# Performance work log

Measured on AMD Instinct MI355X. Metric: run time of the kernel, lower is better.

## Reference

```python
import jax, jax.numpy as jnp
import numpy as np
import math

NUM_BUCKETS = 32
MAX_DISTANCE = 128
NUM_HEADS = 16
D_MODEL = 1024
HEAD_DIM = D_MODEL // NUM_HEADS


def _relative_position_bucket(relative_position, num_buckets=NUM_BUCKETS, max_distance=MAX_DISTANCE):
    # bidirectional=False path of the original
    rp = -jnp.minimum(relative_position, 0)  # non-negative distances
    max_exact = num_buckets // 2
    is_small = rp < max_exact
    rp_safe = jnp.maximum(rp, 1).astype(jnp.float32)
    rp_if_large = max_exact + (
        jnp.log(rp_safe / max_exact) / math.log(max_distance / max_exact) * (num_buckets - max_exact)
    ).astype(jnp.int32)
    rp_if_large = jnp.minimum(rp_if_large, num_buckets - 1)
    return jnp.where(is_small, rp, rp_if_large)


def relative_bias(rab_weight, q_len, k_len):
    ctx = jnp.arange(q_len)[:, None]
    mem = jnp.arange(k_len)[None, :]
    buckets = _relative_position_bucket(mem - ctx)  # [Q, K]
    vals = rab_weight[buckets]                       # [Q, K, H]
    return jnp.transpose(vals, (2, 0, 1))[None]      # [1, H, Q, K]


def setup_inputs() -> dict:
    key = jax.random.key(0)
    k1, k2, k3, k4 = jax.random.split(key, 4)
    B, S = 4, 2048
    return {
        "v": jax.random.normal(k1, (B, S, D_MODEL), dtype=jnp.float32),
        "k": jax.random.normal(k2, (B, S, D_MODEL), dtype=jnp.float32),
        "q": jax.random.normal(k3, (B, S, D_MODEL), dtype=jnp.float32),
        "rab_weight": jax.random.normal(k4, (NUM_BUCKETS, NUM_HEADS), dtype=jnp.float32),
    }


def reference(v, k, q, rab_weight):
    B, S, _ = q.shape
    def split(x):
        return jnp.transpose(x.reshape(B, S, NUM_HEADS, HEAD_DIM), (0, 2, 1, 3))  # [B,H,S,D]
    qh, kh, vh = split(q), split(k), split(v)
    scores = jnp.einsum("bhqd,bhkd->bhqk", qh, kh)          # [B,H,S,S]
    scores = scores + relative_bias(rab_weight, S, S)        # add relative bias
    av = jnp.einsum("bhqk,bhkd->bhqd", jax.nn.silu(scores), vh)
    return jnp.transpose(av, (0, 2, 1, 3)).reshape(B, S, D_MODEL)
```

## Files before the change

### kernel.cpp

```cpp
#include <hip/hip_runtime.h>

#define SEQ 2048
#define NH 16
#define HD 64
#define DMODEL 1024

typedef short bf16x8 __attribute__((ext_vector_type(8)));
typedef float f32x16 __attribute__((ext_vector_type(16)));

union FragU {
    bf16x8 v;
    uint2 u2[2];
    unsigned int w[4];
    unsigned short s[8];
};

#if __has_builtin(__builtin_amdgcn_cvt_pk_bf16_f32)
typedef __bf16 v2bf_t __attribute__((ext_vector_type(2)));
__device__ __forceinline__ unsigned int pack_bf16(float lo, float hi) {
    union { v2bf_t h; unsigned int u; } cv;
    cv.h = __builtin_amdgcn_cvt_pk_bf16_f32(lo, hi);
    return cv.u;
}
#else
__device__ __forceinline__ unsigned int pack_bf16(float lo, float hi) {
    unsigned int a = __float_as_uint(lo) + 0x8000u;
    unsigned int b = __float_as_uint(hi) + 0x8000u;
    return __builtin_amdgcn_perm(b, a, 0x07060302);
}
#endif

#define EXP_SCALE 1.44269504f
#define LN2       0.69314718f

__global__ __launch_bounds__(512, 4)
void paa_kernel(const float* __restrict__ Vg, const float* __restrict__ Kg,
                const float* __restrict__ Qg, const float* __restrict__ RW,
                float* __restrict__ Og)
{
    __shared__ __align__(16) unsigned short KsLds[2][64 * 68];
    __shared__ __align__(16) unsigned short VtLds[2][64 * 68];
    __shared__ float btab[128];

    const int tid  = threadIdx.x;
    const int lane = tid & 63;
    const int wave = tid >> 6;
    const int half = lane >> 5;
    const int l31  = lane & 31;

    const int bid  = blockIdx.x;
    const int bh   = bid & 63;
    const int qt   = bid >> 6;
    const int b    = bh >> 4;
    const int head = bh & 15;

    const int q0w = qt * 256 + wave * 32;

    if (tid < 128) {
        int rp = tid;
        int bucket;
        if (rp < 16) bucket = rp;
        else {
            int big = 16 + (int)(logf((float)rp * 0.0625f) * 7.6943736f);
            bucket = big < 31 ? big : 31;
        }
        btab[tid] = RW[bucket * NH + head] * EXP_SCALE;
    }

    FragU qf[4];
    {
        const float* qrow = Qg + (size_t)(b * SEQ + q0w + l31) * DMODEL + head * HD;
        #pragma unroll
        for (int kf = 0; kf < 4; ++kf) {
            int dd = kf * 16 + half * 8;
            float4 x0 = *(const float4*)(qrow + dd);
            float4 x1 = *(const float4*)(qrow + dd + 4);
            FragU f;
            f.w[0] = pack_bf16(x0.x * EXP_SCALE, x0.y * EXP_SCALE);
            f.w[1] = pack_bf16(x0.z * EXP_SCALE, x0.w * EXP_SCALE);
            f.w[2] = pack_bf16(x1.x * EXP_SCALE, x1.y * EXP_SCALE);
            f.w[3] = pack_bf16(x1.z * EXP_SCALE, x1.w * EXP_SCALE);
            qf[kf] = f;
        }
    }

    f32x16 oacc[2];
    #pragma unroll
    for (int n = 0; n < 2; ++n)
        #pragma unroll
        for (int r = 0; r < 16; ++r) oacc[n][r] = 0.0f;

    const int krow = tid >> 4;
    const int c4   = tid & 15;
    const int kc2  = tid >> 4;
    const int d4   = tid & 15;

    const float* kp = Kg + (size_t)(b * SEQ + krow) * DMODEL + head * HD + c4 * 4;
    const float* vp = Vg + (size_t)(b * SEQ + kc2 * 2) * DMODEL + head * HD + d4 * 4;

    {
        float4 k0 = *(const float4*)(kp);
        float4 k1 = *(const float4*)(kp + (size_t)32 * DMODEL);
        float4 v0 = *(const float4*)(vp);
        float4 v1 = *(const float4*)(vp + DMODEL);
        kp += (size_t)64 * DMODEL;
        vp += (size_t)64 * DMODEL;
        uint2 w;
        w.x = pack_bf16(k0.x, k0.y); w.y = pack_bf16(k0.z, k0.w);
        *(uint2*)&KsLds[0][krow * 68 + c4 * 4] = w;
        w.x = pack_bf16(k1.x, k1.y); w.y = pack_bf16(k1.z, k1.w);
        *(uint2*)&KsLds[0][(krow + 32) * 68 + c4 * 4] = w;
        *(unsigned int*)&VtLds[0][(d4 * 4 + 0) * 68 + kc2 * 2] = pack_bf16(v0.x, v1.x);
        *(unsigned int*)&VtLds[0][(d4 * 4 + 1) * 68 + kc2 * 2] = pack_bf16(v0.y, v1.y);
        *(unsigned int*)&VtLds[0][(d4 * 4 + 2) * 68 + kc2 * 2] = pack_bf16(v0.z, v1.z);
        *(unsigned int*)&VtLds[0][(d4 * 4 + 3) * 68 + kc2 * 2] = pack_bf16(v0.w, v1.w);
    }
    __syncthreads();

    const float bias_d0  = btab[0];
    const float bias_far = btab[127];

    #pragma unroll 2
    for (int it = 0; it < 32; ++it) {
        const int cur = it & 1;
        const int kcb = it * 64;
        const unsigned short* Ks = KsLds[cur];
        const unsigned short* Vt = VtLds[cur];
        const bool pre = (it < 31);

        float4 k0, k1, v0, v1;
        if (pre) {
            k0 = *(const float4*)(kp);
            k1 = *(const float4*)(kp + (size_t)32 * DMODEL);
            v0 = *(const float4*)(vp);
            v1 = *(const float4*)(vp + DMODEL);
            kp += (size_t)64 * DMODEL;
            vp += (size_t)64 * DMODEL;
        }

        f32x16 st[2];
        #pragma unroll
        for (int t = 0; t < 2; ++t) {
            const int kcmin = kcb + t * 32;
            if (q0w + 31 - kcmin <= 0) {
                #pragma unroll
                for (int r = 0; r < 16; ++r) st[t][r] = bias_d0;
            } else if (q0w - (kcmin + 31) >= 113) {
                #pragma unroll
                for (int r = 0; r < 16; ++r) st[t][r] = bias_far;
            } else {
                const int dql = q0w + l31 - kcmin - 4 * half;
                #pragma unroll
                for (int r = 0; r < 16; ++r) {
                    int dv = dql - ((r & 3) + 8 * (r >> 2));
                    dv = dv < 0 ? 0 : (dv > 127 ? 127 : dv);
                    st[t][r] = btab[dv];
                }
            }
        }

        __builtin_amdgcn_s_setprio(1);
        #pragma unroll
        for (int kf = 0; kf < 4; ++kf) {
            FragU ka0, ka1;
            {
                int off = l31 * 68 + kf * 16 + half * 8;
                ka0.u2[0] = *(const uint2*)&Ks[off];
                ka0.u2[1] = *(const uint2*)&Ks[off + 4];
                off += 32 * 68;
                ka1.u2[0] = *(const uint2*)&Ks[off];
                ka1.u2[1] = *(const uint2*)&Ks[off + 4];
            }
            st[0] = __builtin_amdgcn_mfma_f32_32x32x16_bf16(ka0.v, qf[kf].v, st[0], 0, 0, 0);
            st[1] = __builtin_amdgcn_mfma_f32_32x32x16_bf16(ka1.v, qf[kf].v, st[1], 0, 0, 0);
        }
        __builtin_amdgcn_s_setprio(0);

        FragU pf0, pf1, pf2, pf3;
        {
            float vals[16];
            #pragma unroll
            for (int r = 0; r < 16; ++r) {
                float x = st[0][r];
                float e = __builtin_amdgcn_exp2f(-x);
                vals[r] = x * __builtin_amdgcn_rcpf(1.0f + e);
            }
            #pragma unroll
            for (int j = 0; j < 4; ++j) pf0.w[j] = pack_bf16(vals[2 * j], vals[2 * j + 1]);
            #pragma unroll
            for (int j = 0; j < 4; ++j) pf1.w[j] = pack_bf16(vals[8 + 2 * j], vals[9 + 2 * j]);
        }
        #pragma unroll
        for (int n = 0; n < 2; ++n) {
            FragU vf;
            int off = (n * 32 + l31) * 68 + half * 4;
            vf.u2[0] = *(const uint2*)&Vt[off];
            vf.u2[1] = *(const uint2*)&Vt[off + 8];
            oacc[n] = __builtin_amdgcn_mfma_f32_32x32x16_bf16(pf0.v, vf.v, oacc[n], 0, 0, 0);
        }
        #pragma unroll
        for (int n = 0; n < 2; ++n) {
            FragU vf;
            int off = (n * 32 + l31) * 68 + 16 + half * 4;
            vf.u2[0] = *(const uint2*)&Vt[off];
            vf.u2[1] = *(const uint2*)&Vt[off + 8];
            oacc[n] = __builtin_amdgcn_mfma_f32_32x32x16_bf16(pf1.v, vf.v, oacc[n], 0, 0, 0);
        }

        if (pre) {
            const int nb = cur ^ 1;
            uint2 w;
            w.x = pack_bf16(k0.x, k0.y); w.y = pack_bf16(k0.z, k0.w);
            *(uint2*)&KsLds[nb][krow * 68 + c4 * 4] = w;
            w.x = pack_bf16(k1.x, k1.y); w.y = pack_bf16(k1.z, k1.w);
            *(uint2*)&KsLds[nb][(krow + 32) * 68 + c4 * 4] = w;
            *(unsigned int*)&VtLds[nb][(d4 * 4 + 0) * 68 + kc2 * 2] = pack_bf16(v0.x, v1.x);
            *(unsigned int*)&VtLds[nb][(d4 * 4 + 1) * 68 + kc2 * 2] = pack_bf16(v0.y, v1.y);
            *(unsigned int*)&VtLds[nb][(d4 * 4 + 2) * 68 + kc2 * 2] = pack_bf16(v0.z, v1.z);
            *(unsigned int*)&VtLds[nb][(d4 * 4 + 3) * 68 + kc2 * 2] = pack_bf16(v0.w, v1.w);
        }

        {
            float vals[16];
            #pragma unroll
            for (int r = 0; r < 16; ++r) {
                float x = st[1][r];
                float e = __builtin_amdgcn_exp2f(-x);
                vals[r] = x * __builtin_amdgcn_rcpf(1.0f + e);
            }
            #pragma unroll
            for (int j = 0; j < 4; ++j) pf2.w[j] = pack_bf16(vals[2 * j], vals[2 * j + 1]);
            #pragma unroll
            for (int j = 0; j < 4; ++j) pf3.w[j] = pack_bf16(vals[8 + 2 * j], vals[9 + 2 * j]);
        }
        #pragma unroll
        for (int n = 0; n < 2; ++n) {
            FragU vf;
            int off = (n * 32 + l31) * 68 + 32 + half * 4;
            vf.u2[0] = *(const uint2*)&Vt[off];
            vf.u2[1] = *(const uint2*)&Vt[off + 8];
            oacc[n] = __builtin_amdgcn_mfma_f32_32x32x16_bf16(pf2.v, vf.v, oacc[n], 0, 0, 0);
        }
        #pragma unroll
        for (int n = 0; n < 2; ++n) {
            FragU vf;
            int off = (n * 32 + l31) * 68 + 48 + half * 4;
            vf.u2[0] = *(const uint2*)&Vt[off];
            vf.u2[1] = *(const uint2*)&Vt[off + 8];
            oacc[n] = __builtin_amdgcn_mfma_f32_32x32x16_bf16(pf3.v, vf.v, oacc[n], 0, 0, 0);
        }

        if (pre) __syncthreads();
    }

    float* obase = Og + (size_t)(b * SEQ) * DMODEL + head * HD;
    #pragma unroll
    for (int r = 0; r < 16; ++r) {
        int q = q0w + (r & 3) + 8 * (r >> 2) + 4 * half;
        float* orow = obase + (size_t)q * DMODEL;
        #pragma unroll
        for (int n = 0; n < 2; ++n)
            orow[n * 32 + l31] = oacc[n][r] * LN2;
    }
}

extern "C" void kernel_launch(void* const* d_in, const int* in_sizes, int n_in,
                              void* d_out, int out_size, void* d_ws, size_t ws_size,
                              hipStream_t stream) {
    const float* v  = (const float*)d_in[0];
    const float* k  = (const float*)d_in[1];
    const float* q  = (const float*)d_in[2];
    const float* rw = (const float*)d_in[3];
    float* out = (float*)d_out;
    paa_kernel<<<dim3(512), dim3(512), 0, stream>>>(v, k, q, rw, out);
}
```

Baseline: 219.8 us.

## Software-pipeline second score half across iterations with triple-buffered V tiles

Defers the SiLU and PV MFMAs for the second 32-key half of each tile to the start of the next iteration. A third V LDS buffer keeps the previous tile's V alive for that deferred work, and the barrier moves earlier. The aim is to overlap the QK MFMAs with the elementwise SiLU work and cut the serial dependency within an iteration. In exchange it uses more LDS and carries an extra accumulator across iterations, which may raise register pressure at the 512x4 launch bounds.

```diff
diff --git a/kernel.cpp b/kernel.cpp
--- a/kernel.cpp
+++ b/kernel.cpp
@@ -39,7 +39,7 @@
                 float* __restrict__ Og)
 {
     __shared__ __align__(16) unsigned short KsLds[2][64 * 68];
-    __shared__ __align__(16) unsigned short VtLds[2][64 * 68];
+    __shared__ __align__(16) unsigned short VtLds[3][64 * 68];
     __shared__ float btab[128];
 
     const int tid  = threadIdx.x;
@@ -120,12 +120,17 @@
     const float bias_d0  = btab[0];
     const float bias_far = btab[127];
 
+    const unsigned short* Kc = KsLds[0];
+    unsigned short*       Kn = &KsLds[1][0];
+    const unsigned short* Vprev = VtLds[2];
+    const unsigned short* Vc = VtLds[0];
+    unsigned short*       Vn = &VtLds[1][0];
+
+    f32x16 s1c;
+
     #pragma unroll 2
     for (int it = 0; it < 32; ++it) {
-        const int cur = it & 1;
         const int kcb = it * 64;
-        const unsigned short* Ks = KsLds[cur];
-        const unsigned short* Vt = VtLds[cur];
         const bool pre = (it < 31);
 
         float4 k0, k1, v0, v1;
@@ -138,23 +143,55 @@
             vp += (size_t)64 * DMODEL;
         }
 
-        f32x16 st[2];
+        if (it > 0) {
+            float vals[16];
+            #pragma unroll
+            for (int r = 0; r < 16; ++r) {
+                float x = s1c[r];
+                float e = __builtin_amdgcn_exp2f(-x);
+                vals[r] = x * __builtin_amdgcn_rcpf(1.0f + e);
+            }
+            FragU pfA, pfB;
+            #pragma unroll
+            for (int j = 0; j < 4; ++j) pfA.w[j] = pack_bf16(vals[2 * j], vals[2 * j + 1]);
+            #pragma unroll
+            for (int j = 0; j < 4; ++j) pfB.w[j] = pack_bf16(vals[8 + 2 * j], vals[9 + 2 * j]);
+            #pragma unroll
+            for (int n = 0; n < 2; ++n) {
+                FragU vf;
+                int off = (n * 32 + l31) * 68 + 32 + half * 4;
+                vf.u2[0] = *(const uint2*)&Vprev[off];
+                vf.u2[1] = *(const uint2*)&Vprev[off + 8];
+                oacc[n] = __builtin_amdgcn_mfma_f32_32x32x16_bf16(pfA.v, vf.v, oacc[n], 0, 0, 0);
+            }
+            #pragma unroll
+            for (int n = 0; n < 2; ++n) {
+                FragU vf;
+                int off = (n * 32 + l31) * 68 + 48 + half * 4;
+                vf.u2[0] = *(const uint2*)&Vprev[off];
+                vf.u2[1] = *(const uint2*)&Vprev[off + 8];
+                oacc[n] = __builtin_amdgcn_mfma_f32_32x32x16_bf16(pfB.v, vf.v, oacc[n], 0, 0, 0);
+            }
+        }
+
+        f32x16 s0;
         #pragma unroll
         for (int t = 0; t < 2; ++t) {
+            f32x16& st = t ? s1c : s0;
             const int kcmin = kcb + t * 32;
             if (q0w + 31 - kcmin <= 0) {
                 #pragma unroll
-                for (int r = 0; r < 16; ++r) st[t][r] = bias_d0;
+                for (int r = 0; r < 16; ++r) st[r] = bias_d0;
             } else if (q0w - (kcmin + 31) >= 113) {
                 #pragma unroll
-                for (int r = 0; r < 16; ++r) st[t][r] = bias_far;
+                for (int r = 0; r < 16; ++r) st[r] = bias_far;
             } else {
                 const int dql = q0w + l31 - kcmin - 4 * half;
                 #pragma unroll
                 for (int r = 0; r < 16; ++r) {
                     int dv = dql - ((r & 3) + 8 * (r >> 2));
                     dv = dv < 0 ? 0 : (dv > 127 ? 127 : dv);
-                    st[t][r] = btab[dv];
+                    st[r] = btab[dv];
                 }
             }
         }
@@ -165,92 +202,97 @@
             FragU ka0, ka1;
             {
                 int off = l31 * 68 + kf * 16 + half * 8;
-                ka0.u2[0] = *(const uint2*)&Ks[off];
-                ka0.u2[1] = *(const uint2*)&Ks[off + 4];
+                ka0.u2[0] = *(const uint2*)&Kc[off];
+                ka0.u2[1] = *(const uint2*)&Kc[off + 4];
                 off += 32 * 68;
-                ka1.u2[0] = *(const uint2*)&Ks[off];
-                ka1.u2[1] = *(const uint2*)&Ks[off + 4];
-            }
-            st[0] = __builtin_amdgcn_mfma_f32_32x32x16_bf16(ka0.v, qf[kf].v, st[0], 0, 0, 0);
-            st[1] = __builtin_amdgcn_mfma_f32_32x32x16_bf16(ka1.v, qf[kf].v, st[1], 0, 0, 0);
+                ka1.u2[0] = *(const uint2*)&Kc[off];
+                ka1.u2[1] = *(const uint2*)&Kc[off + 4];
+            }
+            s0  = __builtin_amdgcn_mfma_f32_32x32x16_bf16(ka0.v, qf[kf].v, s0,  0, 0, 0);
+            s1c = __builtin_amdgcn_mfma_f32_32x32x16_bf16(ka1.v, qf[kf].v, s1c, 0, 0, 0);
         }
         __builtin_amdgcn_s_setprio(0);
 
-        FragU pf0, pf1, pf2, pf3;
         {
             float vals[16];
             #pragma unroll
             for (int r = 0; r < 16; ++r) {
-                float x = st[0][r];
+                float x = s0[r];
                 float e = __builtin_amdgcn_exp2f(-x);
                 vals[r] = x * __builtin_amdgcn_rcpf(1.0f + e);
             }
+            FragU pf0, pf1;
             #pragma unroll
             for (int j = 0; j < 4; ++j) pf0.w[j] = pack_bf16(vals[2 * j], vals[2 * j + 1]);
             #pragma unroll
             for (int j = 0; j < 4; ++j) pf1.w[j] = pack_bf16(vals[8 + 2 * j], vals[9 + 2 * j]);
-        }
-        #pragma unroll
-        for (int n = 0; n < 2; ++n) {
-            FragU vf;
-            int off = (n * 32 + l31) * 68 + half * 4;
-            vf.u2[0] = *(const uint2*)&Vt[off];
-            vf.u2[1] = *(const uint2*)&Vt[off + 8];
-            oacc[n] = __builtin_amdgcn_mfma_f32_32x32x16_bf16(pf0.v, vf.v, oacc[n], 0, 0, 0);
-        }
-        #pragma unroll
-        for (int n = 0; n < 2; ++n) {
-            FragU vf;
-            int off = (n * 32 + l31) * 68 + 16 + half * 4;
-            vf.u2[0] = *(const uint2*)&Vt[off];
-            vf.u2[1] = *(const uint2*)&Vt[off + 8];
-            oacc[n] = __builtin_amdgcn_mfma_f32_32x32x16_bf16(pf1.v, vf.v, oacc[n], 0, 0, 0);
+            #pragma unroll
+            for (int n = 0; n < 2; ++n) {
+                FragU vf;
+                int off = (n * 32 + l31) * 68 + half * 4;
+                vf.u2[0] = *(const uint2*)&Vc[off];
+                vf.u2[1] = *(const uint2*)&Vc[off + 8];
+                oacc[n] = __builtin_amdgcn_mfma_f32_32x32x16_bf16(pf0.v, vf.v, oacc[n], 0, 0, 0);
+            }
+            #pragma unroll
+            for (int n = 0; n < 2; ++n) {
+                FragU vf;
+                int off = (n * 32 + l31) * 68 + 16 + half * 4;
+                vf.u2[0] = *(const uint2*)&Vc[off];
+                vf.u2[1] = *(const uint2*)&Vc[off + 8];
+                oacc[n] = __builtin_amdgcn_mfma_f32_32x32x16_bf16(pf1.v, vf.v, oacc[n], 0, 0, 0);
+            }
         }
 
         if (pre) {
-            const int nb = cur ^ 1;
             uint2 w;
             w.x = pack_bf16(k0.x, k0.y); w.y = pack_bf16(k0.z, k0.w);
-            *(uint2*)&KsLds[nb][krow * 68 + c4 * 4] = w;
+            *(uint2*)&Kn[krow * 68 + c4 * 4] = w;
             w.x = pack_bf16(k1.x, k1.y); w.y = pack_bf16(k1.z, k1.w);
-            *(uint2*)&KsLds[nb][(krow + 32) * 68 + c4 * 4] = w;
-            *(unsigned int*)&VtLds[nb][(d4 * 4 + 0) * 68 + kc2 * 2] = pack_bf16(v0.x, v1.x);
-            *(unsigned int*)&VtLds[nb][(d4 * 4 + 1) * 68 + kc2 * 2] = pack_bf16(v0.y, v1.y);
-            *(unsigned int*)&VtLds[nb][(d4 * 4 + 2) * 68 + kc2 * 2] = pack_bf16(v0.z, v1.z);
-            *(unsigned int*)&VtLds[nb][(d4 * 4 + 3) * 68 + kc2 * 2] = pack_bf16(v0.w, v1.w);
-        }
+            *(uint2*)&Kn[(krow + 32) * 68 + c4 * 4] = w;
+            *(unsigned int*)&Vn[(d4 * 4 + 0) * 68 + kc2 * 2] = pack_bf16(v0.x, v1.x);
+            *(unsigned int*)&Vn[(d4 * 4 + 1) * 68 + kc2 * 2] = pack_bf16(v0.y, v1.y);
+            *(unsigned int*)&Vn[(d4 * 4 + 2) * 68 + kc2 * 2] = pack_bf16(v0.z, v1.z);
+            *(unsigned int*)&Vn[(d4 * 4 + 3) * 68 + kc2 * 2] = pack_bf16(v0.w, v1.w);
+        }
+
+        if (pre) __syncthreads();
 
         {
-            float vals[16];
-            #pragma unroll
-            for (int r = 0; r < 16; ++r) {
-                float x = st[1][r];
-                float e = __builtin_amdgcn_exp2f(-x);
-                vals[r] = x * __builtin_amdgcn_rcpf(1.0f + e);
-            }
-            #pragma unroll
-            for (int j = 0; j < 4; ++j) pf2.w[j] = pack_bf16(vals[2 * j], vals[2 * j + 1]);
-            #pragma unroll
-            for (int j = 0; j < 4; ++j) pf3.w[j] = pack_bf16(vals[8 + 2 * j], vals[9 + 2 * j]);
-        }
+            const unsigned short* tk = Kc; Kc = Kn; Kn = (unsigned short*)tk;
+            const unsigned short* tv = Vprev; Vprev = Vc; Vc = Vn; Vn = (unsigned short*)tv;
+        }
+    }
+
+    {
+        float vals[16];
+        #pragma unroll
+        for (int r = 0; r < 16; ++r) {
+            float x = s1c[r];
+            float e = __builtin_amdgcn_exp2f(-x);
+            vals[r] = x * __builtin_amdgcn_rcpf(1.0f + e);
+        }
+        FragU pfA, pfB;
+        #pragma unroll
+        for (int j = 0; j < 4; ++j) pfA.w[j] = pack_bf16(vals[2 * j], vals[2 * j + 1]);
+        #pragma unroll
+        for (int j = 0; j < 4; ++j) pfB.w[j] = pack_bf16(vals[8 + 2 * j], vals[9 + 2 * j]);
         #pragma unroll
         for (int n = 0; n < 2; ++n) {
             FragU vf;
             int off = (n * 32 + l31) * 68 + 32 + half * 4;
-            vf.u2[0] = *(const uint2*)&Vt[off];
-            vf.u2[1] = *(const uint2*)&Vt[off + 8];
-            oacc[n] = __builtin_amdgcn_mfma_f32_32x32x16_bf16(pf2.v, vf.v, oacc[n], 0, 0, 0);
+            vf.u2[0] = *(const uint2*)&Vprev[off];
+            vf.u2[1] = *(const uint2*)&Vprev[off + 8];
+            oacc[n] = __builtin_amdgcn_mfma_f32_32x32x16_bf16(pfA.v, vf.v, oacc[n], 0, 0, 0);
         }
         #pragma unroll
         for (int n = 0; n < 2; ++n) {
             FragU vf;
             int off = (n * 32 + l31) * 68 + 48 + half * 4;
-            vf.u2[0] = *(const uint2*)&Vt[off];
-            vf.u2[1] = *(const uint2*)&Vt[off + 8];
-            oacc[n] = __builtin_amdgcn_mfma_f32_32x32x16_bf16(pf3.v, vf.v, oacc[n], 0, 0, 0);
-        }
-
-        if (pre) __syncthreads();
+            vf.u2[0] = *(const uint2*)&Vprev[off];
+            vf.u2[1] = *(const uint2*)&Vprev[off + 8];
+            oacc[n] = __builtin_amdgcn_mfma_f32_32x32x16_bf16(pfB.v, vf.v, oacc[n], 0, 0, 0);
+        }
     }
 
     float* obase = Og + (size_t)(b * SEQ) * DMODEL + head * HD;
```

Measured after the change: 305.5 us. +39.0%, slower.
